# Optimization experiments

Measured on AMD Instinct MI355X. Metric: run time of the kernel, lower is better.

Reference implementation:

```python
import jax, jax.numpy as jnp
import numpy as np

MESH_RESOLUTION = 0.1
ORDER = 3  # TSC interpolation


def setup_inputs() -> dict:
    key = jax.random.key(0)
    k1, k2 = jax.random.split(key)
    L = 20.0
    N, C = 100000, 8
    positions = jax.random.uniform(k1, (N, 3), dtype=jnp.float32) * L
    cell = jnp.eye(3, dtype=jnp.float32) * L
    embeddings = jax.random.normal(k2, (N, C), dtype=jnp.float32)
    return {"positions": positions, "cell": cell, "embeddings": embeddings}


def _weights_order3(dist):
    # dist: [N,3]; returns [3,N,3]
    d2 = dist * dist
    return jnp.stack([
        0.125 * (1.0 - 4.0 * dist + 4.0 * d2),
        0.25 * (3.0 - 4.0 * d2),
        0.125 * (1.0 + 4.0 * dist + 4.0 * d2),
    ])


def reference(positions, cell, embeddings):
    # Mesh setup (cubic box)
    mesh_size = float(jnp.trace(cell)) / 3.0
    n_mesh = int(2 * round(mesh_size / (2.0 * MESH_RESOLUTION)))
    spacing = mesh_size / n_mesh
    C = embeddings.shape[1]

    positions_cell = positions / spacing  # [N,3]
    # odd order: nearest-grid-point centering
    idx = jnp.round(positions_cell).astype(jnp.int32)  # [N,3]
    dist = positions_cell - idx.astype(positions_cell.dtype)  # [N,3]

    w = _weights_order3(dist)  # [3,N,3]
    offs = jnp.arange(1 - (ORDER + 1) // 2, 1 + ORDER // 2)  # [-1,0,1]
    rp = (idx[None, :, :] + offs[:, None, None]) % n_mesh  # [3,N,3]

    xs, ys, zs = jnp.meshgrid(jnp.arange(ORDER), jnp.arange(ORDER), jnp.arange(ORDER), indexing='ij')
    xs, ys, zs = xs.ravel(), ys.ravel(), zs.ravel()  # [27]

    # flat grid indices and combined weights per (corner, atom)
    flat_idx = (rp[xs, :, 0] * n_mesh + rp[ys, :, 1]) * n_mesh + rp[zs, :, 2]  # [27,N]
    wprod = w[xs, :, 0] * w[ys, :, 1] * w[zs, :, 2]  # [27,N]

    vals = wprod[:, :, None] * embeddings[None, :, :]  # [27,N,C]
    grid = jnp.zeros((n_mesh ** 3, C), dtype=positions.dtype)
    grid = grid.at[flat_idx.reshape(-1)].add(vals.reshape(-1, C))
    # -> (C, n, n, n) to match mesh.values layout
    return grid.reshape(n_mesh, n_mesh, n_mesh, C).transpose(3, 0, 1, 2)
```

## Files before the change

### kernel.cpp

```cpp
#include <hip/hip_runtime.h>
#include <math.h>


#define KColCAP 16

typedef float nfloat4 __attribute__((ext_vector_type(4)));

__device__ __forceinline__ float tsc_w(int o, float d) {
    float t = 0.5f + (float)o * d;
    return (o == 0) ? (0.75f - d * d) : (0.5f * t * t);
}

__device__ __forceinline__ float inv_spacing(const float* __restrict__ cell, int n) {
    float tr = cell[0] + cell[4] + cell[8];
    return (3.0f * (float)n) / tr;
}


__global__ __launch_bounds__(256) void fill_recs(
    const float* __restrict__ pos, const float* __restrict__ cell,
    const float* __restrict__ emb,
    int* __restrict__ counts, int* __restrict__ ovf_cnt,
    float4* __restrict__ binrec, int* __restrict__ ovf,
    int N, int n)
{
    int i = blockIdx.x * blockDim.x + threadIdx.x;
    if (i >= N) return;
    float inv_sp = inv_spacing(cell, n);
    float px = pos[3 * i + 0] * inv_sp;
    float py = pos[3 * i + 1] * inv_sp;
    float pz = pos[3 * i + 2] * inv_sp;
    int cx = (int)rintf(px); if (cx >= n) cx -= n; else if (cx < 0) cx += n;
    int cy = (int)rintf(py); if (cy >= n) cy -= n; else if (cy < 0) cy += n;
    int bin = cx * n + cy;
    int slot = atomicAdd(&counts[bin], 1);
    if (slot < KColCAP) {
        const float4* e4 = (const float4*)(emb + (size_t)i * 8);
        float4* r = binrec + (size_t)(bin * KColCAP + slot) * 3;
        r[0] = make_float4(px, py, pz, 0.0f);
        r[1] = e4[0];
        r[2] = e4[1];
    } else {
        int o = atomicAdd(ovf_cnt, 1);
        ovf[o] = i;
    }
}


__global__ __launch_bounds__(256) void gather_col(
    const float4* __restrict__ binrec, const int* __restrict__ counts,
    float* __restrict__ out, int n, int nzc)
{
    const int lane = threadIdx.x & 63;
    const int y = blockIdx.x * 4 + (threadIdx.x >> 6);
    const int x = blockIdx.y;
    if (lane >= nzc) return;
    const int z0 = lane * 4;
    const int half = n >> 1;

    int cnt[3][3], cb[3][3];
    #pragma unroll
    for (int jx = 0; jx < 3; ++jx) {
        int xb = x + jx - 1; if (xb < 0) xb += n; else if (xb >= n) xb -= n;
        #pragma unroll
        for (int jy = 0; jy < 3; ++jy) {
            int yb = y + jy - 1; if (yb < 0) yb += n; else if (yb >= n) yb -= n;
            int bin = xb * n + yb;
            cb[jx][jy] = bin * KColCAP;
            int c = counts[bin];
            cnt[jx][jy] = (c < KColCAP) ? c : KColCAP;
        }
    }

    float acc[4][8];
    #pragma unroll
    for (int zk = 0; zk < 4; ++zk)
        #pragma unroll
        for (int ch = 0; ch < 8; ++ch) acc[zk][ch] = 0.0f;

    #pragma unroll
    for (int jx = 0; jx < 3; ++jx) {
        #pragma unroll
        for (int jy = 0; jy < 3; ++jy) {
            const int c = cnt[jx][jy];
            const float4* rb = binrec + (size_t)cb[jx][jy] * 3;
            for (int s = 0; s < c; ++s) {
                float4 P  = rb[3 * s + 0];
                float4 e0 = rb[3 * s + 1];
                float4 e1 = rb[3 * s + 2];

                float cxf = rintf(P.x); float dx = P.x - cxf;
                float cyf = rintf(P.y); float dy = P.y - cyf;
                float czf = rintf(P.z); float dz = P.z - czf;
                int cz = (int)czf; if (cz >= n) cz -= n; else if (cz < 0) cz += n;

                float tx = 0.5f + (float)(1 - jx) * dx;
                float wx = (jx == 1) ? (0.75f - dx * dx) : (0.5f * tx * tx);
                float ty = 0.5f + (float)(1 - jy) * dy;
                float wy = (jy == 1) ? (0.75f - dy * dy) : (0.5f * ty * ty);
                float wxy = wx * wy;

                #pragma unroll
                for (int zk = 0; zk < 4; ++zk) {
                    int dzi = z0 + zk - cz;
                    if (dzi > half) dzi -= n; else if (dzi < -half) dzi += n;
                    float fd = (float)dzi;
                    float t = 0.5f + fd * dz;
                    float wz = (dzi == 0) ? (0.75f - dz * dz) : (0.5f * t * t);
                    float w = (fabsf(fd) <= 1.0f) ? wxy * wz : 0.0f;
                    acc[zk][0] += w * e0.x;
                    acc[zk][1] += w * e0.y;
                    acc[zk][2] += w * e0.z;
                    acc[zk][3] += w * e0.w;
                    acc[zk][4] += w * e1.x;
                    acc[zk][5] += w * e1.y;
                    acc[zk][6] += w * e1.z;
                    acc[zk][7] += w * e1.w;
                }
            }
        }
    }

    const size_t n3 = (size_t)n * n * n;
    const size_t colbase = ((size_t)x * n + y) * (size_t)n + z0;
    #pragma unroll
    for (int ch = 0; ch < 8; ++ch) {
        nfloat4 v = { acc[0][ch], acc[1][ch], acc[2][ch], acc[3][ch] };
        __builtin_nontemporal_store(v, (nfloat4*)(out + (size_t)ch * n3 + colbase));
    }
}

__global__ __launch_bounds__(256) void deposit_overflow(
    const float* __restrict__ pos, const float* __restrict__ cell,
    const float* __restrict__ emb, const int* __restrict__ ovf_cnt,
    const int* __restrict__ ovf, float* __restrict__ out, int n)
{
    int m = *ovf_cnt;
    int i = blockIdx.x * blockDim.x + threadIdx.x;
    if (i >= m) return;
    int ai = ovf[i];
    float inv_sp = inv_spacing(cell, n);
    float p[3], d[3]; int c0[3];
    #pragma unroll
    for (int kk = 0; kk < 3; ++kk) {
        p[kk] = pos[3 * ai + kk] * inv_sp;
        c0[kk] = (int)rintf(p[kk]);
        d[kk] = p[kk] - (float)c0[kk];
    }
    float w[3][3];
    #pragma unroll
    for (int kk = 0; kk < 3; ++kk) {
        float dd = d[kk];
        w[kk][0] = tsc_w(-1, dd); w[kk][1] = tsc_w(0, dd); w[kk][2] = tsc_w(1, dd);
    }
    int W[3][3];
    #pragma unroll
    for (int kk = 0; kk < 3; ++kk)
        #pragma unroll
        for (int a = 0; a < 3; ++a) {
            int v = c0[kk] - 1 + a; if (v < 0) v += n; else if (v >= n) v -= n;
            W[kk][a] = v;
        }
    size_t n3 = (size_t)n * n * n;
    const float4* e4 = (const float4*)(emb + (size_t)ai * 8);
    float4 e0 = e4[0], e1 = e4[1];
    float e[8] = {e0.x, e0.y, e0.z, e0.w, e1.x, e1.y, e1.z, e1.w};
    for (int a = 0; a < 3; ++a)
        for (int bq = 0; bq < 3; ++bq)
            for (int cq = 0; cq < 3; ++cq) {
                float wt = w[0][a] * w[1][bq] * w[2][cq];
                size_t g = ((size_t)W[0][a] * n + W[1][bq]) * n + W[2][cq];
                #pragma unroll
                for (int ch = 0; ch < 8; ++ch)
                    atomicAdd(out + (size_t)ch * n3 + g, wt * e[ch]);
            }
}


__global__ __launch_bounds__(256) void deposit_tsc8_ilv(
    const float* __restrict__ pos,
    const float* __restrict__ cell,
    const float* __restrict__ emb,
    float* __restrict__ ws,
    int total, int n)
{
    int t = blockIdx.x * blockDim.x + threadIdx.x;
    if (t >= total) return;
    int atom = t / 27;
    int c    = t - atom * 27;
    int a    = c / 9;
    int rem  = c - a * 9;
    int b    = rem / 3;
    int cc   = rem - b * 3;

    float inv_sp = inv_spacing(cell, n);

    float px = pos[3 * atom + 0] * inv_sp;
    float py = pos[3 * atom + 1] * inv_sp;
    float pz = pos[3 * atom + 2] * inv_sp;

    int cx = (int)rintf(px);  float dx = px - (float)cx;
    int cy = (int)rintf(py);  float dy = py - (float)cy;
    int cz = (int)rintf(pz);  float dz = pz - (float)cz;

    float w = tsc_w(a - 1, dx) * tsc_w(b - 1, dy) * tsc_w(cc - 1, dz);

    int x = cx - 1 + a;  if (x < 0) x += n; else if (x >= n) x -= n;
    int y = cy - 1 + b;  if (y < 0) y += n; else if (y >= n) y -= n;
    int z = cz - 1 + cc; if (z < 0) z += n; else if (z >= n) z -= n;

    const float4* e4 = (const float4*)(emb + (size_t)atom * 8);
    float4 e0 = e4[0], e1 = e4[1];

    float* p = ws + ((size_t)((x * n + y) * n + z)) * 8;
    atomicAdd(p + 0, w * e0.x);
    atomicAdd(p + 1, w * e0.y);
    atomicAdd(p + 2, w * e0.z);
    atomicAdd(p + 3, w * e0.w);
    atomicAdd(p + 4, w * e1.x);
    atomicAdd(p + 5, w * e1.y);
    atomicAdd(p + 6, w * e1.z);
    atomicAdd(p + 7, w * e1.w);
}

__global__ __launch_bounds__(256) void transpose_ilv8(
    const float* __restrict__ ws, float* __restrict__ out, int n3)
{
    int t = blockIdx.x * blockDim.x + threadIdx.x;
    int g0 = t * 4;
    if (g0 >= n3) return;
    const float4* w4 = (const float4*)(ws + (size_t)g0 * 8);
    float4 r0 = w4[0], r1 = w4[1];
    float4 r2 = w4[2], r3 = w4[3];
    float4 r4 = w4[4], r5 = w4[5];
    float4 r6 = w4[6], r7 = w4[7];

    *(float4*)(out + (size_t)0 * n3 + g0) = make_float4(r0.x, r2.x, r4.x, r6.x);
    *(float4*)(out + (size_t)1 * n3 + g0) = make_float4(r0.y, r2.y, r4.y, r6.y);
    *(float4*)(out + (size_t)2 * n3 + g0) = make_float4(r0.z, r2.z, r4.z, r6.z);
    *(float4*)(out + (size_t)3 * n3 + g0) = make_float4(r0.w, r2.w, r4.w, r6.w);
    *(float4*)(out + (size_t)4 * n3 + g0) = make_float4(r1.x, r3.x, r5.x, r7.x);
    *(float4*)(out + (size_t)5 * n3 + g0) = make_float4(r1.y, r3.y, r5.y, r7.y);
    *(float4*)(out + (size_t)6 * n3 + g0) = make_float4(r1.z, r3.z, r5.z, r7.z);
    *(float4*)(out + (size_t)7 * n3 + g0) = make_float4(r1.w, r3.w, r5.w, r7.w);
}


__global__ __launch_bounds__(256) void deposit_tsc_gen(
    const float* __restrict__ pos,
    const float* __restrict__ cell,
    const float* __restrict__ emb,
    float* __restrict__ out,
    int N, int n, int C)
{
    int i = blockIdx.x * blockDim.x + threadIdx.x;
    if (i >= N) return;

    float inv_sp = inv_spacing(cell, n);

    float p[3], d[3];
    int c0[3];
    #pragma unroll
    for (int k = 0; k < 3; ++k) {
        p[k] = pos[3 * i + k] * inv_sp;
        c0[k] = (int)rintf(p[k]);
        d[k] = p[k] - (float)c0[k];
    }
    float w[3][3];
    #pragma unroll
    for (int k = 0; k < 3; ++k) {
        float dd = d[k], d2 = dd * dd;
        w[k][0] = 0.125f * (1.0f - 4.0f * dd + 4.0f * d2);
        w[k][1] = 0.25f  * (3.0f - 4.0f * d2);
        w[k][2] = 0.125f * (1.0f + 4.0f * dd + 4.0f * d2);
    }
    int W[3][3];
    #pragma unroll
    for (int k = 0; k < 3; ++k) {
        #pragma unroll
        for (int a = 0; a < 3; ++a) {
            int v = c0[k] - 1 + a; if (v < 0) v += n; else if (v >= n) v -= n;
            W[k][a] = v;
        }
    }
    int n3 = n * n * n;
    for (int a = 0; a < 3; ++a)
        for (int b = 0; b < 3; ++b)
            for (int cc = 0; cc < 3; ++cc) {
                float wt = w[0][a] * w[1][b] * w[2][cc];
                int g = (W[0][a] * n + W[1][b]) * n + W[2][cc];
                for (int ch = 0; ch < C; ++ch)
                    atomicAdd(out + (size_t)ch * n3 + g, wt * emb[(size_t)i * C + ch]);
            }
}

extern "C" void kernel_launch(void* const* d_in, const int* in_sizes, int n_in,
                              void* d_out, int out_size, void* d_ws, size_t ws_size,
                              hipStream_t stream) {
    const float* pos  = (const float*)d_in[0];
    const float* cell = (const float*)d_in[1];
    const float* emb  = (const float*)d_in[2];
    float* out = (float*)d_out;
    float* ws  = (float*)d_ws;

    int N = in_sizes[0] / 3;
    int C = in_sizes[2] / N;
    long long n3l = (long long)out_size / C;
    int n = (int)llroundf(cbrtf((float)n3l));
    int n3 = (int)n3l;

    int block = 256;

    {
        int nb = n * n;
        size_t rec_off = (((size_t)nb + 4 + (size_t)N) * sizeof(int) + 15) & ~(size_t)15;
        size_t need = rec_off + (size_t)nb * KColCAP * 48;
        bool ok = (C == 8) && (n % 4 == 0) && n >= 8 && n <= 256
                  && ws_size >= need
                  && ((long long)n * n * n == n3l);
        if (ok) {
            int* counts  = (int*)d_ws;
            int* ovf_cnt = counts + nb;
            int* ovf     = counts + nb + 4;
            float4* binrec = (float4*)((char*)d_ws + rec_off);

            (void)hipMemsetAsync(counts, 0, (size_t)(nb + 4) * sizeof(int), stream);
            fill_recs<<<(N + block - 1) / block, block, 0, stream>>>(
                pos, cell, emb, counts, ovf_cnt, binrec, ovf, N, n);

            dim3 grid(n / 4, n);
            gather_col<<<grid, block, 0, stream>>>(
                binrec, counts, out, n, n / 4);

            deposit_overflow<<<(N + block - 1) / block, block, 0, stream>>>(
                pos, cell, emb, ovf_cnt, ovf, out, n);
            return;
        }
    }

    size_t need = (size_t)out_size * sizeof(float);
    if (C == 8 && ws_size >= need && (n3 % 4) == 0) {
        (void)hipMemsetAsync(d_ws, 0, need, stream);
        int total = N * 27;
        deposit_tsc8_ilv<<<(total + block - 1) / block, block, 0, stream>>>(
            pos, cell, emb, ws, total, n);
        int tthreads = n3 / 4;
        transpose_ilv8<<<(tthreads + block - 1) / block, block, 0, stream>>>(
            ws, out, n3);
    } else {
        (void)hipMemsetAsync(d_out, 0, (size_t)out_size * sizeof(float), stream);
        int grid = (N + block - 1) / block;
        deposit_tsc_gen<<<grid, block, 0, stream>>>(pos, cell, emb, out, N, n, C);
    }
}
```

Before: 170.7 us.

## Replace per-lane column gather with cooperative LDS atomic scatter per column

The per-column kernel no longer has every z-lane loop over all particles in the 3x3 neighbouring bins and evaluate masked weights. Each wave now splits the particle list across lanes (21 particles times 3 z offsets per pass) and scatters weighted embeddings into an LDS column buffer with shared-memory atomics. The buffer is then streamed to global memory. This cuts the redundant weight evaluation across z-lanes, at the cost of LDS atomic contention, 8 KB of LDS per wave, and a block-wide barrier.

```diff
diff --git a/kernel.cpp b/kernel.cpp
--- a/kernel.cpp
+++ b/kernel.cpp
@@ -47,86 +47,98 @@
 }
 
 
-__global__ __launch_bounds__(256) void gather_col(
+__global__ __launch_bounds__(256) void gather_scatter(
     const float4* __restrict__ binrec, const int* __restrict__ counts,
-    float* __restrict__ out, int n, int nzc)
-{
-    const int lane = threadIdx.x & 63;
-    const int y = blockIdx.x * 4 + (threadIdx.x >> 6);
+    float* __restrict__ out, int n)
+{
+    extern __shared__ float lds[];
+    const int tid = threadIdx.x;
+    const int lane = tid & 63;
+    const int wv = tid >> 6;
+    const int y = blockIdx.x * 4 + wv;
     const int x = blockIdx.y;
-    if (lane >= nzc) return;
+    float* col = lds + wv * 8 * n;
+
+    {
+        nfloat4* c4 = (nfloat4*)col;
+        const int z4 = 2 * n;
+        for (int i = lane; i < z4; i += 64)
+            c4[i] = (nfloat4)(0.f);
+    }
+
+    int base[9], pref[10];
+    pref[0] = 0;
+    #pragma unroll
+    for (int j = 0; j < 9; ++j) {
+        int jx = j / 3, jy = j - 3 * (j / 3);
+        int xb = x + jx - 1; if (xb < 0) xb += n; else if (xb >= n) xb -= n;
+        int yb = y + jy - 1; if (yb < 0) yb += n; else if (yb >= n) yb -= n;
+        int bin = xb * n + yb;
+        base[j] = bin * KColCAP;
+        int c = counts[bin];
+        c = (c < KColCAP) ? c : KColCAP;
+        pref[j + 1] = pref[j] + c;
+    }
+    const int tot = pref[9];
+
+    const int s  = lane / 3;
+    const int zc = lane - 3 * s - 1;
+
+    for (int q0 = 0; q0 < tot; q0 += 21) {
+        const int q = q0 + s;
+        if (s < 21 && q < tot) {
+            int rec = base[0] + q;
+            int jxv = 0, jyv = 0;
+            #pragma unroll
+            for (int k = 1; k < 9; ++k) {
+                bool ge = (q >= pref[k]);
+                int cand = base[k] + (q - pref[k]);
+                rec = ge ? cand : rec;
+                jxv = ge ? (k / 3) : jxv;
+                jyv = ge ? (k - 3 * (k / 3)) : jyv;
+            }
+            const float4* rp = binrec + (size_t)rec * 3;
+            float4 P  = rp[0];
+            float4 e0 = rp[1];
+            float4 e1 = rp[2];
+
+            float cxf = rintf(P.x); float dx = P.x - cxf;
+            float cyf = rintf(P.y); float dy = P.y - cyf;
+            float czf = rintf(P.z); float dz = P.z - czf;
+
+            float tx = 0.5f + (float)(1 - jxv) * dx;
+            float wx = (jxv == 1) ? (0.75f - dx * dx) : (0.5f * tx * tx);
+            float ty = 0.5f + (float)(1 - jyv) * dy;
+            float wy = (jyv == 1) ? (0.75f - dy * dy) : (0.5f * ty * ty);
+            float tz = 0.5f + (float)zc * dz;
+            float wz = (zc == 0) ? (0.75f - dz * dz) : (0.5f * tz * tz);
+            float w = wx * wy * wz;
+
+            int cz = (int)czf; if (cz >= n) cz -= n; else if (cz < 0) cz += n;
+            int z = cz + zc; if (z < 0) z += n; else if (z >= n) z -= n;
+
+            float* p = col + z;
+            atomicAdd(p + 0 * n, w * e0.x);
+            atomicAdd(p + 1 * n, w * e0.y);
+            atomicAdd(p + 2 * n, w * e0.z);
+            atomicAdd(p + 3 * n, w * e0.w);
+            atomicAdd(p + 4 * n, w * e1.x);
+            atomicAdd(p + 5 * n, w * e1.y);
+            atomicAdd(p + 6 * n, w * e1.z);
+            atomicAdd(p + 7 * n, w * e1.w);
+        }
+    }
+    __syncthreads();
+
     const int z0 = lane * 4;
-    const int half = n >> 1;
-
-    int cnt[3][3], cb[3][3];
-    #pragma unroll
-    for (int jx = 0; jx < 3; ++jx) {
-        int xb = x + jx - 1; if (xb < 0) xb += n; else if (xb >= n) xb -= n;
+    if (z0 < n) {
+        const size_t n3 = (size_t)n * n * n;
+        const size_t colbase = ((size_t)x * n + y) * (size_t)n + z0;
         #pragma unroll
-        for (int jy = 0; jy < 3; ++jy) {
-            int yb = y + jy - 1; if (yb < 0) yb += n; else if (yb >= n) yb -= n;
-            int bin = xb * n + yb;
-            cb[jx][jy] = bin * KColCAP;
-            int c = counts[bin];
-            cnt[jx][jy] = (c < KColCAP) ? c : KColCAP;
-        }
-    }
-
-    float acc[4][8];
-    #pragma unroll
-    for (int zk = 0; zk < 4; ++zk)
-        #pragma unroll
-        for (int ch = 0; ch < 8; ++ch) acc[zk][ch] = 0.0f;
-
-    #pragma unroll
-    for (int jx = 0; jx < 3; ++jx) {
-        #pragma unroll
-        for (int jy = 0; jy < 3; ++jy) {
-            const int c = cnt[jx][jy];
-            const float4* rb = binrec + (size_t)cb[jx][jy] * 3;
-            for (int s = 0; s < c; ++s) {
-                float4 P  = rb[3 * s + 0];
-                float4 e0 = rb[3 * s + 1];
-                float4 e1 = rb[3 * s + 2];
-
-                float cxf = rintf(P.x); float dx = P.x - cxf;
-                float cyf = rintf(P.y); float dy = P.y - cyf;
-                float czf = rintf(P.z); float dz = P.z - czf;
-                int cz = (int)czf; if (cz >= n) cz -= n; else if (cz < 0) cz += n;
-
-                float tx = 0.5f + (float)(1 - jx) * dx;
-                float wx = (jx == 1) ? (0.75f - dx * dx) : (0.5f * tx * tx);
-                float ty = 0.5f + (float)(1 - jy) * dy;
-                float wy = (jy == 1) ? (0.75f - dy * dy) : (0.5f * ty * ty);
-                float wxy = wx * wy;
-
-                #pragma unroll
-                for (int zk = 0; zk < 4; ++zk) {
-                    int dzi = z0 + zk - cz;
-                    if (dzi > half) dzi -= n; else if (dzi < -half) dzi += n;
-                    float fd = (float)dzi;
-                    float t = 0.5f + fd * dz;
-                    float wz = (dzi == 0) ? (0.75f - dz * dz) : (0.5f * t * t);
-                    float w = (fabsf(fd) <= 1.0f) ? wxy * wz : 0.0f;
-                    acc[zk][0] += w * e0.x;
-                    acc[zk][1] += w * e0.y;
-                    acc[zk][2] += w * e0.z;
-                    acc[zk][3] += w * e0.w;
-                    acc[zk][4] += w * e1.x;
-                    acc[zk][5] += w * e1.y;
-                    acc[zk][6] += w * e1.z;
-                    acc[zk][7] += w * e1.w;
-                }
-            }
-        }
-    }
-
-    const size_t n3 = (size_t)n * n * n;
-    const size_t colbase = ((size_t)x * n + y) * (size_t)n + z0;
-    #pragma unroll
-    for (int ch = 0; ch < 8; ++ch) {
-        nfloat4 v = { acc[0][ch], acc[1][ch], acc[2][ch], acc[3][ch] };
-        __builtin_nontemporal_store(v, (nfloat4*)(out + (size_t)ch * n3 + colbase));
+        for (int ch = 0; ch < 8; ++ch) {
+            nfloat4 v = *(const nfloat4*)(col + ch * n + z0);
+            __builtin_nontemporal_store(v, (nfloat4*)(out + (size_t)ch * n3 + colbase));
+        }
     }
 }
 
@@ -313,9 +325,11 @@
 
     {
         int nb = n * n;
+        size_t lds_bytes = (size_t)4 * 8 * n * sizeof(float);
         size_t rec_off = (((size_t)nb + 4 + (size_t)N) * sizeof(int) + 15) & ~(size_t)15;
         size_t need = rec_off + (size_t)nb * KColCAP * 48;
         bool ok = (C == 8) && (n % 4 == 0) && n >= 8 && n <= 256
+                  && lds_bytes <= 64 * 1024
                   && ws_size >= need
                   && ((long long)n * n * n == n3l);
         if (ok) {
@@ -329,8 +343,8 @@
                 pos, cell, emb, counts, ovf_cnt, binrec, ovf, N, n);
 
             dim3 grid(n / 4, n);
-            gather_col<<<grid, block, 0, stream>>>(
-                binrec, counts, out, n, n / 4);
+            gather_scatter<<<grid, block, lds_bytes, stream>>>(
+                binrec, counts, out, n);
 
             deposit_overflow<<<(N + block - 1) / block, block, 0, stream>>>(
                 pos, cell, emb, ovf_cnt, ovf, out, n);
```

Result: faster. 145.9 us (-14.5%).
